# Optimization experiments

Hardware: AMD Instinct MI355X
Metric: run time of the kernel (lower is better)

Reference implementation:

```python
import jax, jax.numpy as jnp
import numpy as np

H, D = 8, 128           # num_heads, head_dim
HID = 1024              # hidden_size
K = 4                   # short conv kernel
EPS_QK = 1e-6
EPS_NORM = 1e-5


def short_conv(x, w):
    # x: (B, T, C), w: (C, 1, K) depthwise causal conv (zero initial state) + SiLU
    k = w.shape[-1]
    xp = jnp.pad(x, ((0, 0), (k - 1, 0), (0, 0)))
    xc = jnp.transpose(xp, (0, 2, 1))  # (B, C, T+K-1)
    y = jax.lax.conv_general_dilated(xc, w, window_strides=(1,), padding='VALID',
                                     feature_group_count=w.shape[0])
    return jax.nn.silu(jnp.transpose(y, (0, 2, 1)))


def _rmsn(t, eps):
    return t * jax.lax.rsqrt(jnp.mean(t * t, axis=-1, keepdims=True) + eps)


def setup_inputs() -> dict:
    key = jax.random.key(0)
    ks = jax.random.split(key, 16)
    s = 0.02
    inp = {
        'x': jax.random.normal(ks[0], (2, 1024, HID), dtype=jnp.float32),
        'Wq': jax.random.normal(ks[1], (H * D, HID), dtype=jnp.float32) * s,
        'Wk': jax.random.normal(ks[2], (H * D, HID), dtype=jnp.float32) * s,
        'Wv': jax.random.normal(ks[3], (H * D, HID), dtype=jnp.float32) * s,
        'wq_conv': jax.random.normal(ks[4], (H * D, 1, K), dtype=jnp.float32) * 0.3,
        'wk_conv': jax.random.normal(ks[5], (H * D, 1, K), dtype=jnp.float32) * 0.3,
        'wv_conv': jax.random.normal(ks[6], (H * D, 1, K), dtype=jnp.float32) * 0.3,
        'Wfa': jax.random.normal(ks[7], (D, HID), dtype=jnp.float32) * s,
        'Wfb': jax.random.normal(ks[8], (H * D, D), dtype=jnp.float32) * s,
        'Wb': jax.random.normal(ks[9], (H, HID), dtype=jnp.float32) * s,
        'Wga': jax.random.normal(ks[10], (D, HID), dtype=jnp.float32) * s,
        'Wgb': jax.random.normal(ks[11], (H * D, D), dtype=jnp.float32) * s,
        'A_log': jnp.log(jax.random.uniform(ks[12], (H,), minval=1.0, maxval=16.0, dtype=jnp.float32)),
        'dt_bias': jnp.zeros((H, D), dtype=jnp.float32),
        'o_norm_w': jnp.ones((D,), dtype=jnp.float32),
        'Wo': jax.random.normal(ks[13], (HID, H * D), dtype=jnp.float32) * s,
    }
    return inp


def reference(x, Wq, Wk, Wv, wq_conv, wk_conv, wv_conv, Wfa, Wfb, Wb, Wga, Wgb,
              A_log, dt_bias, o_norm_w, Wo):
    B, T, _ = x.shape
    scale = float(D) ** -0.5

    q = short_conv(x @ Wq.T, wq_conv).reshape(B, T, H, D)
    k = short_conv(x @ Wk.T, wk_conv).reshape(B, T, H, D)
    v = short_conv(x @ Wv.T, wv_conv).reshape(B, T, H, D)

    q = (scale ** 2) * _rmsn(q, EPS_QK)
    k = scale * _rmsn(k, EPS_QK)

    a_logits = ((x @ Wfa.T) @ Wfb.T).reshape(B, T, H, D)
    g = -jnp.exp(A_log)[None, None, :, None] * jax.nn.softplus(a_logits + dt_bias)  # (B,T,H,D)
    beta = jax.nn.sigmoid(x @ Wb.T)  # (B,T,H)

    # gated delta-rule recurrence over time; state S: (B, H, Dk, Dv)
    def step(S, inputs):
        q_t, k_t, v_t, g_t, b_t = inputs
        S = S * jnp.exp(g_t)[..., None]                       # per-channel decay on key dim
        kv = jnp.einsum('bhd,bhdv->bhv', k_t, S)              # read
        delta = b_t[..., None] * (v_t - kv)                   # beta-gated delta
        S = S + k_t[..., None] * delta[:, :, None, :]         # rank-1 write
        o = jnp.einsum('bhd,bhdv->bhv', q_t, S)
        return S, o

    tb = lambda t: jnp.moveaxis(t, 1, 0)  # (B,T,...) -> (T,B,...)
    S0 = jnp.zeros((B, H, D, D), dtype=x.dtype)
    _, o_t = jax.lax.scan(step, S0, (tb(q), tb(k), tb(v), tb(g), tb(beta)))
    out = jnp.moveaxis(o_t, 0, 1)  # (B, T, H, D)

    gate = ((x @ Wga.T) @ Wgb.T).reshape(B, T, H, D)
    out = _rmsn(out, EPS_NORM) * o_norm_w * jax.nn.sigmoid(gate)
    return out.reshape(B, T, H * D) @ Wo.T
```

## Files before the change

### kernel.cpp

```cpp
#include <hip/hip_runtime.h>
#include <hip/hip_bf16.h>
#include <math.h>

#define H 8
#define D 128
#define HID 1024
#define KCONV 4

typedef __bf16 bhalf;
typedef __bf16 bhalf4 __attribute__((ext_vector_type(4)));
typedef __bf16 bhalf8 __attribute__((ext_vector_type(8)));
typedef float f32x4 __attribute__((ext_vector_type(4)));
typedef _Float16 hlf;
typedef _Float16 half8 __attribute__((ext_vector_type(8)));
typedef _Float16 half4v __attribute__((ext_vector_type(4)));

__device__ __forceinline__ void async16(const void* g, void* l) {
    __builtin_amdgcn_global_load_lds(
        (const __attribute__((address_space(1))) void*)g,
        (__attribute__((address_space(3))) void*)l, 16, 0, 0);
}

__global__ __launch_bounds__(256) void gemm_bf16_nt(const bhalf* A, const bhalf* B,
                                                    void* Cv,
                                                    int M, int N, int K,
                                                    int lda, int ldb, int ldc, int epi,
                                                    const float* __restrict__ A_log,
                                                    const float* __restrict__ dt_bias,
                                                    const bhalf* A2, const bhalf* B2,
                                                    void* C2, int epi2,
                                                    bhalf* __restrict__ pXAG,
                                                    float* __restrict__ pBETA)
{
    if (blockIdx.z) { A = A2; B = B2; Cv = C2; epi = epi2; }
    __shared__ __align__(16) bhalf As[128][32];
    __shared__ __align__(16) bhalf Bs[64][32];
    int tid = threadIdx.x;
    int wid = tid >> 6, lane = tid & 63;
    int rowBase = blockIdx.y * 128;
    int colBase = blockIdx.x * 64;
    int wm = wid >> 1, wn = wid & 1;

    f32x4 acc[4][2] = {};

    int r = lane >> 2;
    int cseg = lane & 3;

    for (int k0 = 0; k0 < K; k0 += 32) {
        __syncthreads();
#pragma unroll
        for (int s = 0; s < 3; ++s) {
            int j = wid * 3 + s;
            if (j < 8) {
                const bhalf* ga = A + (size_t)(rowBase + j * 16 + r) * lda + k0 + cseg * 8;
                async16(ga, &As[j * 16][0]);
            } else {
                int jb = j - 8;
                const bhalf* ga = B + (size_t)(colBase + jb * 16 + r) * ldb + k0 + cseg * 8;
                async16(ga, &Bs[jb * 16][0]);
            }
        }
        __syncthreads();
        int mq = lane & 15, kq = (lane >> 4) * 8;
        bhalf8 af[4], bfr[2];
#pragma unroll
        for (int mt = 0; mt < 4; ++mt)
            af[mt] = *(const bhalf8*)&As[wm * 64 + mt * 16 + mq][kq];
#pragma unroll
        for (int nt = 0; nt < 2; ++nt)
            bfr[nt] = *(const bhalf8*)&Bs[wn * 32 + nt * 16 + mq][kq];
#pragma unroll
        for (int mt = 0; mt < 4; ++mt)
#pragma unroll
            for (int nt = 0; nt < 2; ++nt)
                acc[mt][nt] = __builtin_amdgcn_mfma_f32_16x16x32_bf16(
                    af[mt], bfr[nt], acc[mt][nt], 0, 0, 0);
    }
    int rquad = (lane >> 4) * 4;
#pragma unroll
    for (int mt = 0; mt < 4; ++mt) {
        int m0 = rowBase + wm * 64 + mt * 16 + rquad;
#pragma unroll
        for (int nt = 0; nt < 2; ++nt) {
            int c = colBase + wn * 32 + (lane & 15) + nt * 16;
#pragma unroll
            for (int rr = 0; rr < 4; ++rr) {
                float val = acc[mt][nt][rr];
                int m = m0 + rr;
                if (epi == 0) {
                    ((float*)Cv)[(size_t)m * ldc + c] = val;
                } else if (epi == 1) {
                    int h = c >> 7, d = c & 127;
                    float z = val + dt_bias[h * D + d];
                    float sp = (z > 20.f) ? z : log1pf(expf(z));
                    ((float*)Cv)[(size_t)m * ldc + c] = expf(-expf(A_log[h]) * sp);
                } else if (epi == 2) {
                    ((bhalf*)Cv)[(size_t)m * ldc + c] = (bhalf)val;
                } else {
                    if (c < 3072) {
                        ((float*)Cv)[(size_t)m * 3072 + c] = val;
                    } else if (c < 3328) {
                        pXAG[(size_t)m * 256 + (c - 3072)] = (bhalf)val;
                    } else if (c < 3336) {
                        pBETA[(size_t)m * 8 + (c - 3328)] = 1.f / (1.f + expf(-val));
                    }
                }
            }
        }
    }
}

__global__ void cast1(const float* __restrict__ s, bhalf* __restrict__ d, int n4)
{
    int i = blockIdx.x * blockDim.x + threadIdx.x;
    if (i >= n4) return;
    float4 v = ((const float4*)s)[i];
    bhalf4 o = {(bhalf)v.x, (bhalf)v.y, (bhalf)v.z, (bhalf)v.w};
    ((bhalf4*)d)[i] = o;
}
__global__ void cast4(const float* __restrict__ s0, const float* __restrict__ s1,
                      const float* __restrict__ s2, const float* __restrict__ s3,
                      bhalf* __restrict__ d0, bhalf* __restrict__ d1,
                      bhalf* __restrict__ d2, bhalf* __restrict__ d3, int n4)
{
    int i = blockIdx.x * blockDim.x + threadIdx.x;
    if (i >= n4) return;
    int a = blockIdx.y;
    const float* s = (a == 0) ? s0 : (a == 1) ? s1 : (a == 2) ? s2 : s3;
    bhalf* d = (a == 0) ? d0 : (a == 1) ? d1 : (a == 2) ? d2 : d3;
    float4 v = ((const float4*)s)[i];
    bhalf4 o = {(bhalf)v.x, (bhalf)v.y, (bhalf)v.z, (bhalf)v.w};
    ((bhalf4*)d)[i] = o;
}

__global__ __launch_bounds__(128) void conv3_kernel(const float* __restrict__ QKV,
                                                    const float* __restrict__ wq,
                                                    const float* __restrict__ wk,
                                                    const float* __restrict__ wv,
                                                    float* __restrict__ Qc,
                                                    float* __restrict__ Kc,
                                                    float* __restrict__ Vc,
                                                    int T)
{
    int which = blockIdx.y;
    const float* w; float* out; int mode; float scale;
    if (which == 0)      { w = wq; out = Qc; mode = 1; scale = 1.0f / 128.0f; }
    else if (which == 1) { w = wk; out = Kc; mode = 1; scale = 0.08838834764831845f; }
    else                 { w = wv; out = Vc; mode = 0; scale = 1.f; }

    int bid = blockIdx.x;
    int h = bid % H;
    int t = (bid / H) % T;
    int b = bid / (H * T);
    int d = threadIdx.x;
    int c = h * D + d;
    const float* base = QKV + (size_t)b * T * 3072 + which * 1024 + c;
    float acc = 0.f;
#pragma unroll
    for (int j = 0; j < KCONV; ++j) {
        int tt = t - (KCONV - 1) + j;
        float xv = (tt >= 0) ? base[(size_t)tt * 3072] : 0.f;
        acc += xv * w[c * KCONV + j];
    }
    float y = acc / (1.f + expf(-acc));
    if (mode) {
        __shared__ float red[2];
        float ss = y * y;
#pragma unroll
        for (int s = 32; s > 0; s >>= 1) ss += __shfl_xor(ss, s, 64);
        if ((threadIdx.x & 63) == 0) red[threadIdx.x >> 6] = ss;
        __syncthreads();
        float tot = red[0] + red[1];
        float r = rsqrtf(tot * (1.f / D) + 1e-6f);
        y = y * r * scale;
    }
    out[(size_t)bid * D + d] = y;
}

template <int CTRL>
__device__ __forceinline__ float dpp_add(float x) {
    int y = __builtin_amdgcn_update_dpp(0, __builtin_bit_cast(int, x),
                                        CTRL, 0xF, 0xF, false);
    return x + __builtin_bit_cast(float, y);
}
__device__ __forceinline__ float wave_sum63(float x) {
    x = dpp_add<0x111>(x);
    x = dpp_add<0x112>(x);
    x = dpp_add<0x114>(x);
    x = dpp_add<0x118>(x);
    x = dpp_add<0x142>(x);
    x = dpp_add<0x143>(x);
    return x;
}


__global__ __launch_bounds__(256) void chunk_prep_kernel(
    const float* __restrict__ Q, const float* __restrict__ K,
    const float* __restrict__ V, const float* __restrict__ E,
    const float* __restrict__ BETA,
    hlf* __restrict__ Wn, float* __restrict__ Uf, hlf* __restrict__ Qt,
    hlf* __restrict__ AoL, hlf* __restrict__ KbT, float* __restrict__ Aend,
    int T)
{
    __shared__ __align__(16) float e_s[32][128];
    __shared__ __align__(16) float k_s[32][128];
    __shared__ __align__(16) float U_s[32][128];
    __shared__ __align__(16) hlf  A_s[32][128];
    __shared__ __align__(16) hlf  W_s[32][128];
    __shared__ float P_s[32][32];
    __shared__ float Ao_s[32][32];
    __shared__ float beta_s[32];

    int tid = threadIdx.x, wid = tid >> 6, lane = tid & 63;
    int bid = blockIdx.x;
    int bh = bid >> 5, ch = bid & 31;
    int b = bh >> 3, h = bh & 7;
    int t0 = ch * 32;
    size_t rowb = (size_t)(b * T + t0) * 1024 + h * 128;
    size_t co = (size_t)bh * 32 + ch;

    int rs2 = lane >> 5, seg = (lane & 31) * 4;
#pragma unroll
    for (int p = wid * 4; p < wid * 4 + 4; ++p) {
        int row = p * 2 + rs2;
        async16(E + rowb + (size_t)row * 1024 + seg, &e_s[p * 2][0]);
        async16(K + rowb + (size_t)row * 1024 + seg, &k_s[p * 2][0]);
    }
    __syncthreads();

    for (int x = tid; x < 1024; x += 256) Ao_s[x >> 5][x & 31] = 0.f;
    if (wid == 2 && lane < 32)
        beta_s[lane] = BETA[(size_t)(b * T + t0 + lane) * 8 + h];
    int d0 = lane * 2;
    if (wid == 0) {
        float a0 = 1.f, a1 = 1.f;
        for (int t = 0; t < 32; ++t) {
            a0 *= e_s[t][d0]; a1 *= e_s[t][d0 + 1];
            A_s[t][d0] = (hlf)a0; A_s[t][d0 + 1] = (hlf)a1;
        }
        Aend[co * 128 + d0] = a0; Aend[co * 128 + d0 + 1] = a1;
    } else if (wid == 1) {
        float s0 = 1.f, s1 = 1.f;
        for (int t = 31; t >= 0; --t) {
            KbT[co * 4096 + (size_t)d0 * 32 + t]       = (hlf)(k_s[t][d0] * s0);
            KbT[co * 4096 + (size_t)(d0 + 1) * 32 + t] = (hlf)(k_s[t][d0 + 1] * s1);
            s0 *= e_s[t][d0]; s1 *= e_s[t][d0 + 1];
        }
    }
    __syncthreads();

#pragma unroll
    for (int ii = 0; ii < 8; ++ii) {
        int i = wid + ii * 4;
        float ki0 = k_s[i][d0], ki1 = k_s[i][d0 + 1];
        float2 qv = *(const float2*)(Q + rowb + (size_t)i * 1024 + d0);
        float aa = wave_sum63(qv.x * ki0 + qv.y * ki1);
        if (lane == 63) Ao_s[i][i] = aa;
        float R0 = 1.f, R1 = 1.f;
        for (int j = i - 1; j >= 0; --j) {
            R0 *= e_s[j + 1][d0]; R1 *= e_s[j + 1][d0 + 1];
            float u0 = R0 * k_s[j][d0], u1 = R1 * k_s[j][d0 + 1];
            float pp = wave_sum63(ki0 * u0 + ki1 * u1);
            float a2 = wave_sum63(qv.x * u0 + qv.y * u1);
            if (lane == 63) { P_s[i][j] = pp; Ao_s[i][j] = a2; }
        }
    }
    __syncthreads();

    for (int x = tid; x < 1024; x += 256) {
        int i2 = x >> 5, j2 = x & 31;
        P_s[i2][j2] = (j2 < i2) ? P_s[i2][j2] * beta_s[i2] : 0.f;
    }
    __syncthreads();

    if (wid == 0) {
        for (int i = 0; i < 32; ++i) {
            float bb = beta_s[i];
            float a0 = bb * k_s[i][d0] * (float)A_s[i][d0];
            float a1 = bb * k_s[i][d0 + 1] * (float)A_s[i][d0 + 1];
            for (int k2 = 0; k2 < i; ++k2) {
                float L = P_s[i][k2];
                a0 -= L * (float)W_s[k2][d0];
                a1 -= L * (float)W_s[k2][d0 + 1];
            }
            W_s[i][d0] = (hlf)a0; W_s[i][d0 + 1] = (hlf)a1;
        }
    } else if (wid == 1) {
        for (int i = 0; i < 32; ++i) {
            float bb = beta_s[i];
            float2 vv = *(const float2*)(V + rowb + (size_t)i * 1024 + d0);
            float a0 = bb * vv.x, a1 = bb * vv.y;
            for (int k2 = 0; k2 < i; ++k2) {
                float L = P_s[i][k2];
                a0 -= L * U_s[k2][d0];
                a1 -= L * U_s[k2][d0 + 1];
            }
            U_s[i][d0] = a0; U_s[i][d0 + 1] = a1;
        }
    } else {
        for (int r2 = wid - 2; r2 < 32; r2 += 2) {
            float2 qv = *(const float2*)(Q + rowb + (size_t)r2 * 1024 + d0);
            Qt[co * 4096 + (size_t)r2 * 128 + d0]     = (hlf)(qv.x * (float)A_s[r2][d0]);
            Qt[co * 4096 + (size_t)r2 * 128 + d0 + 1] = (hlf)(qv.y * (float)A_s[r2][d0 + 1]);
        }
    }
    __syncthreads();

    for (int x = tid; x < 4096; x += 256) {
        Wn[co * 4096 + x] = (hlf)(-(float)W_s[x >> 7][x & 127]);
        Uf[co * 4096 + x] = U_s[x >> 7][x & 127];
    }
    for (int x = tid; x < 1024; x += 256)
        AoL[co * 1024 + x] = (hlf)Ao_s[x >> 5][x & 31];
}

__global__ __launch_bounds__(256) void chunk_scan_kernel(
    const hlf* __restrict__ Wn, const float* __restrict__ Uf,
    const hlf* __restrict__ Qt, const hlf* __restrict__ Ao,
    const hlf* __restrict__ KbT, const float* __restrict__ Aend,
    float* __restrict__ O, int T)
{
    __shared__ __align__(16) float Sf[32][132];
    __shared__ __align__(16) hlf  Sh[32][136];
    __shared__ __align__(16) hlf  Dt[32][40];
    __shared__ float Ae[128];

    int tid = threadIdx.x, wid = tid >> 6, lane = tid & 63;
    int nbh = gridDim.x >> 2;
    int bh = blockIdx.x % nbh, vs = blockIdx.x / nbh;
    int b = bh >> 3, h = bh & 7;
    int v0 = vs * 32;

    for (int r = wid; r < 32; r += 4) {
        for (int c2 = lane; c2 < 132; c2 += 64) Sf[r][c2] = 0.f;
        for (int c2 = lane; c2 < 136; c2 += 64) Sh[r][c2] = (hlf)0.f;
    }
    __syncthreads();

    int mq = lane & 15, kq = (lane >> 4) * 8, rq = (lane >> 4) * 4;
    int tr = (wid >> 1) * 16, vc = (wid & 1) * 16;
    int vr2 = (wid >> 1) * 16, dh2 = (wid & 1) * 64;

    for (int c = 0; c < 32; ++c) {
        size_t co = (size_t)bh * 32 + c;
        const hlf*   Wc  = Wn  + co * 4096;
        const float* Uc  = Uf  + co * 4096;
        const hlf*   Qc2 = Qt  + co * 4096;
        const hlf*   Aoc = Ao  + co * 1024;
        const hlf*   Kbc = KbT + co * 4096;
        if (tid < 128) Ae[tid] = Aend[co * 128 + tid];

        f32x4 dacc;
#pragma unroll
        for (int rr = 0; rr < 4; ++rr)
            dacc[rr] = Uc[(size_t)(tr + rq + rr) * 128 + v0 + vc + mq];
#pragma unroll
        for (int ks = 0; ks < 4; ++ks) {
            half8 aw = *(const half8*)&Wc[(size_t)(tr + mq) * 128 + ks * 32 + kq];
            half8 bs = *(const half8*)&Sh[vc + mq][ks * 32 + kq];
            dacc = __builtin_amdgcn_mfma_f32_16x16x32_f16(aw, bs, dacc, 0, 0, 0);
        }
        half4v dh4;
#pragma unroll
        for (int rr = 0; rr < 4; ++rr) dh4[rr] = (hlf)dacc[rr];
        *(half4v*)&Dt[vc + mq][tr + rq] = dh4;
        __syncthreads();

        f32x4 oacc = {0.f, 0.f, 0.f, 0.f};
#pragma unroll
        for (int ks = 0; ks < 4; ++ks) {
            half8 aq = *(const half8*)&Qc2[(size_t)(tr + mq) * 128 + ks * 32 + kq];
            half8 bs = *(const half8*)&Sh[vc + mq][ks * 32 + kq];
            oacc = __builtin_amdgcn_mfma_f32_16x16x32_f16(aq, bs, oacc, 0, 0, 0);
        }
        {
            half8 aA = *(const half8*)&Aoc[(tr + mq) * 32 + kq];
            half8 bD = *(const half8*)&Dt[vc + mq][kq];
            oacc = __builtin_amdgcn_mfma_f32_16x16x32_f16(aA, bD, oacc, 0, 0, 0);
        }
#pragma unroll
        for (int rr = 0; rr < 4; ++rr)
            O[((size_t)(b * T + c * 32 + tr + rq + rr) * 8 + h) * 128 + v0 + vc + mq]
                = oacc[rr];

        f32x4 sacc[4];
        half8 aD = *(const half8*)&Dt[vr2 + mq][kq];
#pragma unroll
        for (int nt = 0; nt < 4; ++nt) {
            int dc = dh2 + nt * 16 + mq;
#pragma unroll
            for (int rr = 0; rr < 4; ++rr)
                sacc[nt][rr] = Sf[vr2 + rq + rr][dc] * Ae[dc];
            half8 bK = *(const half8*)&Kbc[(size_t)dc * 32 + kq];
            sacc[nt] = __builtin_amdgcn_mfma_f32_16x16x32_f16(aD, bK, sacc[nt], 0, 0, 0);
        }
        __syncthreads();
#pragma unroll
        for (int nt = 0; nt < 4; ++nt) {
            int dc = dh2 + nt * 16 + mq;
#pragma unroll
            for (int rr = 0; rr < 4; ++rr) {
                Sf[vr2 + rq + rr][dc] = sacc[nt][rr];
                Sh[vr2 + rq + rr][dc] = (hlf)sacc[nt][rr];
            }
        }
        __syncthreads();
    }
}

__global__ __launch_bounds__(128) void outnorm_kernel(const float* __restrict__ O,
                                                      const float* __restrict__ GATE,
                                                      const float* __restrict__ w,
                                                      bhalf* __restrict__ Obf)
{
    int bid = blockIdx.x;
    int d = threadIdx.x;
    size_t base = (size_t)bid * D;
    float y = O[base + d];
    __shared__ float red[2];
    float ss = y * y;
#pragma unroll
    for (int s = 32; s > 0; s >>= 1) ss += __shfl_xor(ss, s, 64);
    if ((threadIdx.x & 63) == 0) red[threadIdx.x >> 6] = ss;
    __syncthreads();
    float tot = red[0] + red[1];
    float r = rsqrtf(tot * (1.f / D) + 1e-5f);
    float gz = GATE[base + d];
    float sg = 1.f / (1.f + expf(-gz));
    Obf[base + d] = (bhalf)(y * r * w[d] * sg);
}

extern "C" void kernel_launch(void* const* d_in, const int* in_sizes, int n_in,
                              void* d_out, int out_size, void* d_ws, size_t ws_size,
                              hipStream_t stream)
{
    const float* x       = (const float*)d_in[0];
    const float* Wq      = (const float*)d_in[1];
    const float* Wk      = (const float*)d_in[2];
    const float* Wv      = (const float*)d_in[3];
    const float* wq_conv = (const float*)d_in[4];
    const float* wk_conv = (const float*)d_in[5];
    const float* wv_conv = (const float*)d_in[6];
    const float* Wfa     = (const float*)d_in[7];
    const float* Wfb     = (const float*)d_in[8];
    const float* Wb      = (const float*)d_in[9];
    const float* Wga     = (const float*)d_in[10];
    const float* Wgb     = (const float*)d_in[11];
    const float* A_log   = (const float*)d_in[12];
    const float* dt_bias = (const float*)d_in[13];
    const float* o_norm_w= (const float*)d_in[14];
    const float* Wo      = (const float*)d_in[15];

    int BT = in_sizes[0] / HID;
    int T = 1024;
    int B_ = BT / T;
    size_t M = (size_t)BT;
    size_t sz_big = M * HID;
    const int nW = HID * HID;
    const int nS = D * HID;
    const int NCAT = 3392;

    float* fp = (float*)d_ws;
    float* QKVp = fp;               fp += 3 * sz_big;
    float* Qc   = fp;               fp += sz_big;
    float* Kc   = fp;               fp += sz_big;
    float* Vc   = fp;               fp += sz_big;
    float* EGb  = fp;               fp += sz_big;
    float* GATE = fp;               fp += sz_big;
    float* Obuf = fp;               fp += sz_big;
    float* BETA = fp;               fp += M * H;
    bhalf* bp = (bhalf*)fp;
    bhalf* xb   = bp;               bp += sz_big;
    bhalf* Wcat = bp;               bp += (size_t)NCAT * HID;
    bhalf* Wob  = bp;               bp += nW;
    bhalf* Wfbb = bp;               bp += nS;
    bhalf* Wgbb = bp;               bp += nS;
    bhalf* XAG  = bp;               bp += M * 256;
    bhalf* Obf  = bp;               bp += sz_big;

    dim3 blk(256);

    cast1<<<(int)((sz_big / 4 + 255) / 256), 256, 0, stream>>>(x, xb, (int)(sz_big / 4));
    cast4<<<dim3((nW / 4 + 255) / 256, 4), 256, 0, stream>>>(Wq, Wk, Wv, Wo,
        Wcat, Wcat + nW, Wcat + 2 * (size_t)nW, Wob, nW / 4);
    cast4<<<dim3((nS / 4 + 255) / 256, 4), 256, 0, stream>>>(Wfa, Wga, Wfb, Wgb,
        Wcat + 3 * (size_t)nW, Wcat + 3 * (size_t)nW + nS, Wfbb, Wgbb, nS / 4);
    cast1<<<(H * HID / 4 + 255) / 256, 256, 0, stream>>>(Wb,
        Wcat + 3 * (size_t)nW + 2 * (size_t)nS, H * HID / 4);

    gemm_bf16_nt<<<dim3(NCAT / 64, BT / 128), blk, 0, stream>>>(
        xb, Wcat, QKVp, BT, NCAT, HID, HID, HID, 3072, 3, nullptr, nullptr,
        nullptr, nullptr, nullptr, 0, XAG, BETA);

    conv3_kernel<<<dim3(BT * H, 3), 128, 0, stream>>>(QKVp,
                                                      wq_conv, wk_conv, wv_conv,
                                                      Qc, Kc, Vc, T);

    gemm_bf16_nt<<<dim3(HID / 64, BT / 128, 2), blk, 0, stream>>>(
        XAG, Wfbb, EGb, BT, HID, D, 256, D, HID, 1, A_log, dt_bias,
        XAG + D, Wgbb, GATE, 0, nullptr, nullptr);

    int nbh = B_ * 8;
    float* Uf   = QKVp;
    float* Aend = Uf + (size_t)nbh * 32 * 4096;
    hlf* Wn  = (hlf*)(Aend + (size_t)nbh * 32 * 128);
    hlf* Qt  = Wn  + (size_t)nbh * 32 * 4096;
    hlf* AoLp= Qt  + (size_t)nbh * 32 * 4096;
    hlf* KbT = AoLp + (size_t)nbh * 32 * 1024;

    chunk_prep_kernel<<<nbh * 32, 256, 0, stream>>>(Qc, Kc, Vc, EGb, BETA,
                                                    Wn, Uf, Qt, AoLp, KbT, Aend, T);
    chunk_scan_kernel<<<nbh * 4, 256, 0, stream>>>(Wn, Uf, Qt, AoLp, KbT, Aend,
                                                   Obuf, T);

    outnorm_kernel<<<BT * H, 128, 0, stream>>>(Obuf, GATE, o_norm_w, Obf);

    gemm_bf16_nt<<<dim3(HID / 64, BT / 128), blk, 0, stream>>>(
        Obf, Wob, (float*)d_out, BT, HID, HID, HID, HID, HID, 0, nullptr, nullptr,
        nullptr, nullptr, nullptr, 0, nullptr, nullptr);
}
```

Baseline: 331.2 us.

## Prefetch next chunk operands into registers and double-buffer scan state

The chunk scan kernel now loads all global operands for the next chunk into registers while the current chunk computes, and ping-pongs the state between two LDS buffers so one barrier per phase is removed. Barriers become raw s_barrier calls with explicit waitcnt and sched_barrier. The prep kernel also stages Q and V in LDS through async loads instead of reading them from global memory repeatedly. This adds register pressure (launch bounds set to one block per CU) and more LDS use.

```diff
diff --git a/kernel.cpp b/kernel.cpp
--- a/kernel.cpp
+++ b/kernel.cpp
@@ -204,6 +204,8 @@
 {
     __shared__ __align__(16) float e_s[32][128];
     __shared__ __align__(16) float k_s[32][128];
+    __shared__ __align__(16) float q_s[32][128];
+    __shared__ __align__(16) float v_s[32][128];
     __shared__ __align__(16) float U_s[32][128];
     __shared__ __align__(16) hlf  A_s[32][128];
     __shared__ __align__(16) hlf  W_s[32][128];
@@ -225,12 +227,14 @@
         int row = p * 2 + rs2;
         async16(E + rowb + (size_t)row * 1024 + seg, &e_s[p * 2][0]);
         async16(K + rowb + (size_t)row * 1024 + seg, &k_s[p * 2][0]);
-    }
-    __syncthreads();
-
-    for (int x = tid; x < 1024; x += 256) Ao_s[x >> 5][x & 31] = 0.f;
+        async16(Q + rowb + (size_t)row * 1024 + seg, &q_s[p * 2][0]);
+        async16(V + rowb + (size_t)row * 1024 + seg, &v_s[p * 2][0]);
+    }
     if (wid == 2 && lane < 32)
         beta_s[lane] = BETA[(size_t)(b * T + t0 + lane) * 8 + h];
+    __syncthreads();
+
+    for (int x = tid; x < 1024; x += 256) Ao_s[x >> 5][x & 31] = 0.f;
     int d0 = lane * 2;
     if (wid == 0) {
         float a0 = 1.f, a1 = 1.f;
@@ -253,7 +257,7 @@
     for (int ii = 0; ii < 8; ++ii) {
         int i = wid + ii * 4;
         float ki0 = k_s[i][d0], ki1 = k_s[i][d0 + 1];
-        float2 qv = *(const float2*)(Q + rowb + (size_t)i * 1024 + d0);
+        float2 qv = *(const float2*)&q_s[i][d0];
         float aa = wave_sum63(qv.x * ki0 + qv.y * ki1);
         if (lane == 63) Ao_s[i][i] = aa;
         float R0 = 1.f, R1 = 1.f;
@@ -288,7 +292,7 @@
     } else if (wid == 1) {
         for (int i = 0; i < 32; ++i) {
             float bb = beta_s[i];
-            float2 vv = *(const float2*)(V + rowb + (size_t)i * 1024 + d0);
+            float2 vv = *(const float2*)&v_s[i][d0];
             float a0 = bb * vv.x, a1 = bb * vv.y;
             for (int k2 = 0; k2 < i; ++k2) {
                 float L = P_s[i][k2];
@@ -299,7 +303,7 @@
         }
     } else {
         for (int r2 = wid - 2; r2 < 32; r2 += 2) {
-            float2 qv = *(const float2*)(Q + rowb + (size_t)r2 * 1024 + d0);
+            float2 qv = *(const float2*)&q_s[r2][d0];
             Qt[co * 4096 + (size_t)r2 * 128 + d0]     = (hlf)(qv.x * (float)A_s[r2][d0]);
             Qt[co * 4096 + (size_t)r2 * 128 + d0 + 1] = (hlf)(qv.y * (float)A_s[r2][d0 + 1]);
         }
@@ -314,16 +318,123 @@
         AoL[co * 1024 + x] = (hlf)Ao_s[x >> 5][x & 31];
 }
 
-__global__ __launch_bounds__(256) void chunk_scan_kernel(
+struct ScanOps {
+    half8 aw0, aw1, aw2, aw3;
+    half8 aq0, aq1, aq2, aq3;
+    half8 bK0, bK1, bK2, bK3;
+    half8 aA;
+    float u0, u1, u2, u3;
+    float ae0, ae1, ae2, ae3;
+};
+
+__device__ __forceinline__ void scan_load(ScanOps& o, size_t co,
+    const hlf* __restrict__ Wn, const float* __restrict__ Uf,
+    const hlf* __restrict__ Qt, const hlf* __restrict__ Ao,
+    const hlf* __restrict__ KbT, const float* __restrict__ Aend,
+    int tr, int vc, int dh2, int mq, int kq, int rq, int v0)
+{
+    const hlf*   Wc  = Wn  + co * 4096;
+    const hlf*   Qc  = Qt  + co * 4096;
+    const hlf*   Aoc = Ao  + co * 1024;
+    const hlf*   Kbc = KbT + co * 4096;
+    const float* Uc  = Uf  + co * 4096;
+    const float* Aec = Aend + co * 128;
+    size_t rw = (size_t)(tr + mq) * 128 + kq;
+    o.aw0 = *(const half8*)&Wc[rw];
+    o.aw1 = *(const half8*)&Wc[rw + 32];
+    o.aw2 = *(const half8*)&Wc[rw + 64];
+    o.aw3 = *(const half8*)&Wc[rw + 96];
+    o.aq0 = *(const half8*)&Qc[rw];
+    o.aq1 = *(const half8*)&Qc[rw + 32];
+    o.aq2 = *(const half8*)&Qc[rw + 64];
+    o.aq3 = *(const half8*)&Qc[rw + 96];
+    o.aA  = *(const half8*)&Aoc[(tr + mq) * 32 + kq];
+    o.bK0 = *(const half8*)&Kbc[(size_t)(dh2 + mq) * 32 + kq];
+    o.bK1 = *(const half8*)&Kbc[(size_t)(dh2 + 16 + mq) * 32 + kq];
+    o.bK2 = *(const half8*)&Kbc[(size_t)(dh2 + 32 + mq) * 32 + kq];
+    o.bK3 = *(const half8*)&Kbc[(size_t)(dh2 + 48 + mq) * 32 + kq];
+    size_t ru = (size_t)(tr + rq) * 128 + v0 + vc + mq;
+    o.u0 = Uc[ru];
+    o.u1 = Uc[ru + 128];
+    o.u2 = Uc[ru + 256];
+    o.u3 = Uc[ru + 384];
+    o.ae0 = Aec[dh2 + mq];
+    o.ae1 = Aec[dh2 + 16 + mq];
+    o.ae2 = Aec[dh2 + 32 + mq];
+    o.ae3 = Aec[dh2 + 48 + mq];
+}
+
+__device__ __forceinline__ void scan_body(const ScanOps& o, int c,
+    float (*SfR)[132], hlf (*ShR)[136], float (*SfW)[132], hlf (*ShW)[136],
+    hlf (*Dt)[40], float* __restrict__ O,
+    int b, int h, int v0, int T,
+    int tr, int vc, int vr2, int dh2, int mq, int kq, int rq)
+{
+    half8 bs0 = *(const half8*)&ShR[vc + mq][kq];
+    half8 bs1 = *(const half8*)&ShR[vc + mq][32 + kq];
+    half8 bs2 = *(const half8*)&ShR[vc + mq][64 + kq];
+    half8 bs3 = *(const half8*)&ShR[vc + mq][96 + kq];
+
+    f32x4 dacc = {o.u0, o.u1, o.u2, o.u3};
+    dacc = __builtin_amdgcn_mfma_f32_16x16x32_f16(o.aw0, bs0, dacc, 0, 0, 0);
+    dacc = __builtin_amdgcn_mfma_f32_16x16x32_f16(o.aw1, bs1, dacc, 0, 0, 0);
+    dacc = __builtin_amdgcn_mfma_f32_16x16x32_f16(o.aw2, bs2, dacc, 0, 0, 0);
+    dacc = __builtin_amdgcn_mfma_f32_16x16x32_f16(o.aw3, bs3, dacc, 0, 0, 0);
+    half4v dh4 = {(hlf)dacc[0], (hlf)dacc[1], (hlf)dacc[2], (hlf)dacc[3]};
+    *(half4v*)&Dt[vc + mq][tr + rq] = dh4;
+
+    asm volatile("s_waitcnt lgkmcnt(0)" ::: "memory");
+    __builtin_amdgcn_s_barrier();
+    __builtin_amdgcn_sched_barrier(0);
+
+    f32x4 oacc = {0.f, 0.f, 0.f, 0.f};
+    oacc = __builtin_amdgcn_mfma_f32_16x16x32_f16(o.aq0, bs0, oacc, 0, 0, 0);
+    oacc = __builtin_amdgcn_mfma_f32_16x16x32_f16(o.aq1, bs1, oacc, 0, 0, 0);
+    oacc = __builtin_amdgcn_mfma_f32_16x16x32_f16(o.aq2, bs2, oacc, 0, 0, 0);
+    oacc = __builtin_amdgcn_mfma_f32_16x16x32_f16(o.aq3, bs3, oacc, 0, 0, 0);
+    half8 bD = *(const half8*)&Dt[vc + mq][kq];
+    oacc = __builtin_amdgcn_mfma_f32_16x16x32_f16(o.aA, bD, oacc, 0, 0, 0);
+    size_t ob = ((size_t)(b * T + c * 32 + tr + rq) * 8 + h) * 128 + v0 + vc + mq;
+    O[ob]        = oacc[0];
+    O[ob + 1024] = oacc[1];
+    O[ob + 2048] = oacc[2];
+    O[ob + 3072] = oacc[3];
+
+    half8 aD = *(const half8*)&Dt[vr2 + mq][kq];
+    int dc0 = dh2 + mq, dc1 = dh2 + 16 + mq, dc2 = dh2 + 32 + mq, dc3 = dh2 + 48 + mq;
+    f32x4 s0, s1, s2, s3;
+#pragma unroll
+    for (int rr = 0; rr < 4; ++rr) {
+        s0[rr] = SfR[vr2 + rq + rr][dc0] * o.ae0;
+        s1[rr] = SfR[vr2 + rq + rr][dc1] * o.ae1;
+        s2[rr] = SfR[vr2 + rq + rr][dc2] * o.ae2;
+        s3[rr] = SfR[vr2 + rq + rr][dc3] * o.ae3;
+    }
+    s0 = __builtin_amdgcn_mfma_f32_16x16x32_f16(aD, o.bK0, s0, 0, 0, 0);
+    s1 = __builtin_amdgcn_mfma_f32_16x16x32_f16(aD, o.bK1, s1, 0, 0, 0);
+    s2 = __builtin_amdgcn_mfma_f32_16x16x32_f16(aD, o.bK2, s2, 0, 0, 0);
+    s3 = __builtin_amdgcn_mfma_f32_16x16x32_f16(aD, o.bK3, s3, 0, 0, 0);
+#pragma unroll
+    for (int rr = 0; rr < 4; ++rr) {
+        SfW[vr2 + rq + rr][dc0] = s0[rr];  ShW[vr2 + rq + rr][dc0] = (hlf)s0[rr];
+        SfW[vr2 + rq + rr][dc1] = s1[rr];  ShW[vr2 + rq + rr][dc1] = (hlf)s1[rr];
+        SfW[vr2 + rq + rr][dc2] = s2[rr];  ShW[vr2 + rq + rr][dc2] = (hlf)s2[rr];
+        SfW[vr2 + rq + rr][dc3] = s3[rr];  ShW[vr2 + rq + rr][dc3] = (hlf)s3[rr];
+    }
+    asm volatile("s_waitcnt lgkmcnt(0)" ::: "memory");
+    __builtin_amdgcn_s_barrier();
+    __builtin_amdgcn_sched_barrier(0);
+}
+
+__global__ __launch_bounds__(256, 1) void chunk_scan_kernel(
     const hlf* __restrict__ Wn, const float* __restrict__ Uf,
     const hlf* __restrict__ Qt, const hlf* __restrict__ Ao,
     const hlf* __restrict__ KbT, const float* __restrict__ Aend,
     float* __restrict__ O, int T)
 {
-    __shared__ __align__(16) float Sf[32][132];
-    __shared__ __align__(16) hlf  Sh[32][136];
+    __shared__ __align__(16) float Sf0[32][132], Sf1[32][132];
+    __shared__ __align__(16) hlf  Sh0[32][136], Sh1[32][136];
     __shared__ __align__(16) hlf  Dt[32][40];
-    __shared__ float Ae[128];
 
     int tid = threadIdx.x, wid = tid >> 6, lane = tid & 63;
     int nbh = gridDim.x >> 2;
@@ -332,79 +443,30 @@
     int v0 = vs * 32;
 
     for (int r = wid; r < 32; r += 4) {
-        for (int c2 = lane; c2 < 132; c2 += 64) Sf[r][c2] = 0.f;
-        for (int c2 = lane; c2 < 136; c2 += 64) Sh[r][c2] = (hlf)0.f;
-    }
-    __syncthreads();
+        for (int c2 = lane; c2 < 132; c2 += 64) Sf0[r][c2] = 0.f;
+        for (int c2 = lane; c2 < 136; c2 += 64) Sh0[r][c2] = (hlf)0.f;
+    }
 
     int mq = lane & 15, kq = (lane >> 4) * 8, rq = (lane >> 4) * 4;
     int tr = (wid >> 1) * 16, vc = (wid & 1) * 16;
     int vr2 = (wid >> 1) * 16, dh2 = (wid & 1) * 64;
 
-    for (int c = 0; c < 32; ++c) {
-        size_t co = (size_t)bh * 32 + c;
-        const hlf*   Wc  = Wn  + co * 4096;
-        const float* Uc  = Uf  + co * 4096;
-        const hlf*   Qc2 = Qt  + co * 4096;
-        const hlf*   Aoc = Ao  + co * 1024;
-        const hlf*   Kbc = KbT + co * 4096;
-        if (tid < 128) Ae[tid] = Aend[co * 128 + tid];
-
-        f32x4 dacc;
-#pragma unroll
-        for (int rr = 0; rr < 4; ++rr)
-            dacc[rr] = Uc[(size_t)(tr + rq + rr) * 128 + v0 + vc + mq];
-#pragma unroll
-        for (int ks = 0; ks < 4; ++ks) {
-            half8 aw = *(const half8*)&Wc[(size_t)(tr + mq) * 128 + ks * 32 + kq];
-            half8 bs = *(const half8*)&Sh[vc + mq][ks * 32 + kq];
-            dacc = __builtin_amdgcn_mfma_f32_16x16x32_f16(aw, bs, dacc, 0, 0, 0);
-        }
-        half4v dh4;
-#pragma unroll
-        for (int rr = 0; rr < 4; ++rr) dh4[rr] = (hlf)dacc[rr];
-        *(half4v*)&Dt[vc + mq][tr + rq] = dh4;
-        __syncthreads();
-
-        f32x4 oacc = {0.f, 0.f, 0.f, 0.f};
-#pragma unroll
-        for (int ks = 0; ks < 4; ++ks) {
-            half8 aq = *(const half8*)&Qc2[(size_t)(tr + mq) * 128 + ks * 32 + kq];
-            half8 bs = *(const half8*)&Sh[vc + mq][ks * 32 + kq];
-            oacc = __builtin_amdgcn_mfma_f32_16x16x32_f16(aq, bs, oacc, 0, 0, 0);
-        }
-        {
-            half8 aA = *(const half8*)&Aoc[(tr + mq) * 32 + kq];
-            half8 bD = *(const half8*)&Dt[vc + mq][kq];
-            oacc = __builtin_amdgcn_mfma_f32_16x16x32_f16(aA, bD, oacc, 0, 0, 0);
-        }
-#pragma unroll
-        for (int rr = 0; rr < 4; ++rr)
-            O[((size_t)(b * T + c * 32 + tr + rq + rr) * 8 + h) * 128 + v0 + vc + mq]
-                = oacc[rr];
-
-        f32x4 sacc[4];
-        half8 aD = *(const half8*)&Dt[vr2 + mq][kq];
-#pragma unroll
-        for (int nt = 0; nt < 4; ++nt) {
-            int dc = dh2 + nt * 16 + mq;
-#pragma unroll
-            for (int rr = 0; rr < 4; ++rr)
-                sacc[nt][rr] = Sf[vr2 + rq + rr][dc] * Ae[dc];
-            half8 bK = *(const half8*)&Kbc[(size_t)dc * 32 + kq];
-            sacc[nt] = __builtin_amdgcn_mfma_f32_16x16x32_f16(aD, bK, sacc[nt], 0, 0, 0);
-        }
-        __syncthreads();
-#pragma unroll
-        for (int nt = 0; nt < 4; ++nt) {
-            int dc = dh2 + nt * 16 + mq;
-#pragma unroll
-            for (int rr = 0; rr < 4; ++rr) {
-                Sf[vr2 + rq + rr][dc] = sacc[nt][rr];
-                Sh[vr2 + rq + rr][dc] = (hlf)sacc[nt][rr];
-            }
-        }
-        __syncthreads();
+    int NC = T / 32;
+    size_t cb = (size_t)bh * 32;
+    ScanOps opA, opB;
+    scan_load(opA, cb, Wn, Uf, Qt, Ao, KbT, Aend, tr, vc, dh2, mq, kq, rq, v0);
+    __syncthreads();
+
+    for (int cc = 0; cc < NC; cc += 2) {
+        scan_load(opB, cb + cc + 1, Wn, Uf, Qt, Ao, KbT, Aend,
+                  tr, vc, dh2, mq, kq, rq, v0);
+        scan_body(opA, cc, Sf0, Sh0, Sf1, Sh1, Dt, O, b, h, v0, T,
+                  tr, vc, vr2, dh2, mq, kq, rq);
+        if (cc + 2 < NC)
+            scan_load(opA, cb + cc + 2, Wn, Uf, Qt, Ao, KbT, Aend,
+                      tr, vc, dh2, mq, kq, rq, v0);
+        scan_body(opB, cc + 1, Sf1, Sh1, Sf0, Sh0, Dt, O, b, h, v0, T,
+                  tr, vc, vr2, dh2, mq, kq, rq);
     }
 }
 
```

Result: slower. 352.3 us (+6.4%).

## Rewrite chunk scan as single-wave blocks with register state and double-buffered prefetch

Applied to the files above, without the earlier changes.

Rewrites the chunk scan kernel so each block is one wavefront that owns a 16-column slice of the value dimension, raising the grid from 4 to 8 blocks per (batch, head). The fp32 state now lives in registers instead of LDS. Operands for the next two chunks are prefetched with inline-asm global loads and async LDS copies, with manual waitcnt control, removing block-wide barriers from the sequential chunk loop. The output buffer moves to a slice-major layout that outnorm now indexes, and the prep kernel stages V through LDS asynchronously. The cost is heavy register pressure, fragile hand-tuned wait counts, and one wave per block.

```diff
diff --git a/kernel.cpp b/kernel.cpp
--- a/kernel.cpp
+++ b/kernel.cpp
@@ -225,6 +225,7 @@
         int row = p * 2 + rs2;
         async16(E + rowb + (size_t)row * 1024 + seg, &e_s[p * 2][0]);
         async16(K + rowb + (size_t)row * 1024 + seg, &k_s[p * 2][0]);
+        async16(V + rowb + (size_t)row * 1024 + seg, &U_s[p * 2][0]);
     }
     __syncthreads();
 
@@ -288,7 +289,7 @@
     } else if (wid == 1) {
         for (int i = 0; i < 32; ++i) {
             float bb = beta_s[i];
-            float2 vv = *(const float2*)(V + rowb + (size_t)i * 1024 + d0);
+            float2 vv = *(const float2*)&U_s[i][d0];
             float a0 = bb * vv.x, a1 = bb * vv.y;
             for (int k2 = 0; k2 < i; ++k2) {
                 float L = P_s[i][k2];
@@ -314,109 +315,262 @@
         AoL[co * 1024 + x] = (hlf)Ao_s[x >> 5][x & 31];
 }
 
-__global__ __launch_bounds__(256) void chunk_scan_kernel(
+struct ScanOpsA {
+    half8 aw0, aw1, aw2, aw3, aw4, aw5, aw6, aw7;
+    half8 aq0, aq1, aq2, aq3, aq4, aq5, aq6, aq7;
+    half8 aA0, aA1;
+    float u0, u1, u2, u3, u4, u5, u6, u7;
+};
+
+#define GLOAD16(dst, ptr) \
+    asm volatile("global_load_dwordx4 %0, %1, off" : "=v"(dst) : "v"(ptr))
+#define GLOAD4(dst, ptr) \
+    asm volatile("global_load_dword %0, %1, off" : "=v"(dst) : "v"(ptr))
+
+#define SCAN_WAIT35(o) \
+    do { \
+    asm volatile("s_waitcnt vmcnt(35)" \
+        : "+v"(o.aw0), "+v"(o.aw1), "+v"(o.aw2), "+v"(o.aw3), \
+          "+v"(o.aw4), "+v"(o.aw5), "+v"(o.aw6), "+v"(o.aw7), \
+          "+v"(o.aq0), "+v"(o.aq1), "+v"(o.aq2), "+v"(o.aq3), \
+          "+v"(o.aq4), "+v"(o.aq5), "+v"(o.aq6), "+v"(o.aq7) \
+        :: "memory"); \
+    asm volatile("" \
+        : "+v"(o.aA0), "+v"(o.aA1), \
+          "+v"(o.u0), "+v"(o.u1), "+v"(o.u2), "+v"(o.u3), \
+          "+v"(o.u4), "+v"(o.u5), "+v"(o.u6), "+v"(o.u7)); \
+    __builtin_amdgcn_sched_barrier(0); \
+    } while (0)
+
+__device__ __forceinline__ void scan_loadA(ScanOpsA& o, size_t co,
+    const hlf* __restrict__ Wn, const float* __restrict__ Uf,
+    const hlf* __restrict__ Qt, const hlf* __restrict__ Ao,
+    int mq, int kq, int rq, int v0)
+{
+    const hlf*   Wc  = Wn + co * 4096;
+    const hlf*   Qc  = Qt + co * 4096;
+    const hlf*   Aoc = Ao + co * 1024;
+    const float* Uc  = Uf + co * 4096;
+    size_t rw0 = (size_t)mq * 128 + kq;
+    size_t rw1 = (size_t)(16 + mq) * 128 + kq;
+    GLOAD16(o.aw0, &Wc[rw0]);
+    GLOAD16(o.aw1, &Wc[rw0 + 32]);
+    GLOAD16(o.aw2, &Wc[rw0 + 64]);
+    GLOAD16(o.aw3, &Wc[rw0 + 96]);
+    GLOAD16(o.aw4, &Wc[rw1]);
+    GLOAD16(o.aw5, &Wc[rw1 + 32]);
+    GLOAD16(o.aw6, &Wc[rw1 + 64]);
+    GLOAD16(o.aw7, &Wc[rw1 + 96]);
+    GLOAD16(o.aq0, &Qc[rw0]);
+    GLOAD16(o.aq1, &Qc[rw0 + 32]);
+    GLOAD16(o.aq2, &Qc[rw0 + 64]);
+    GLOAD16(o.aq3, &Qc[rw0 + 96]);
+    GLOAD16(o.aq4, &Qc[rw1]);
+    GLOAD16(o.aq5, &Qc[rw1 + 32]);
+    GLOAD16(o.aq6, &Qc[rw1 + 64]);
+    GLOAD16(o.aq7, &Qc[rw1 + 96]);
+    GLOAD16(o.aA0, &Aoc[mq * 32 + kq]);
+    GLOAD16(o.aA1, &Aoc[(16 + mq) * 32 + kq]);
+    size_t ru0 = (size_t)rq * 128 + v0 + mq;
+    size_t ru1 = (size_t)(16 + rq) * 128 + v0 + mq;
+    GLOAD4(o.u0, &Uc[ru0]);
+    GLOAD4(o.u1, &Uc[ru0 + 128]);
+    GLOAD4(o.u2, &Uc[ru0 + 256]);
+    GLOAD4(o.u3, &Uc[ru0 + 384]);
+    GLOAD4(o.u4, &Uc[ru1]);
+    GLOAD4(o.u5, &Uc[ru1 + 128]);
+    GLOAD4(o.u6, &Uc[ru1 + 256]);
+    GLOAD4(o.u7, &Uc[ru1 + 384]);
+}
+
+__device__ __forceinline__ void scan_stage(size_t co,
+    const hlf* __restrict__ KbT, const float* __restrict__ Aend,
+    hlf* kbt_l, float* ae_l, int lane)
+{
+    const hlf* Kbc = KbT + co * 4096;
+#pragma unroll
+    for (int p = 0; p < 8; ++p)
+        async16(Kbc + p * 512 + lane * 8, kbt_l + p * 512);
+    async16(Aend + co * 128 + lane * 4, ae_l);
+}
+
+__device__ __forceinline__ void scan_body(const ScanOpsA& o,
+    const hlf* kbt_l, const float* ae_l, int c,
+    f32x4* sreg, half8* Sb, hlf (*Sh)[136], hlf (*Dt)[40],
+    float* __restrict__ O, int b, int h, int vs, int T, int Mrows,
+    int mq, int kq, int rq)
+{
+    f32x4 d0 = {0.f, 0.f, 0.f, 0.f}, d1 = {0.f, 0.f, 0.f, 0.f};
+    d0 = __builtin_amdgcn_mfma_f32_16x16x32_f16(o.aw0, Sb[0], d0, 0, 0, 0);
+    d0 = __builtin_amdgcn_mfma_f32_16x16x32_f16(o.aw1, Sb[1], d0, 0, 0, 0);
+    d0 = __builtin_amdgcn_mfma_f32_16x16x32_f16(o.aw2, Sb[2], d0, 0, 0, 0);
+    d0 = __builtin_amdgcn_mfma_f32_16x16x32_f16(o.aw3, Sb[3], d0, 0, 0, 0);
+    d1 = __builtin_amdgcn_mfma_f32_16x16x32_f16(o.aw4, Sb[0], d1, 0, 0, 0);
+    d1 = __builtin_amdgcn_mfma_f32_16x16x32_f16(o.aw5, Sb[1], d1, 0, 0, 0);
+    d1 = __builtin_amdgcn_mfma_f32_16x16x32_f16(o.aw6, Sb[2], d1, 0, 0, 0);
+    d1 = __builtin_amdgcn_mfma_f32_16x16x32_f16(o.aw7, Sb[3], d1, 0, 0, 0);
+    d0[0] += o.u0; d0[1] += o.u1; d0[2] += o.u2; d0[3] += o.u3;
+    d1[0] += o.u4; d1[1] += o.u5; d1[2] += o.u6; d1[3] += o.u7;
+    half4v dh0 = {(hlf)d0[0], (hlf)d0[1], (hlf)d0[2], (hlf)d0[3]};
+    half4v dh1 = {(hlf)d1[0], (hlf)d1[1], (hlf)d1[2], (hlf)d1[3]};
+    *(half4v*)&Dt[mq][rq]      = dh0;
+    *(half4v*)&Dt[mq][16 + rq] = dh1;
+
+    f32x4 o0 = {0.f, 0.f, 0.f, 0.f}, o1 = {0.f, 0.f, 0.f, 0.f};
+    o0 = __builtin_amdgcn_mfma_f32_16x16x32_f16(o.aq0, Sb[0], o0, 0, 0, 0);
+    o0 = __builtin_amdgcn_mfma_f32_16x16x32_f16(o.aq1, Sb[1], o0, 0, 0, 0);
+    o0 = __builtin_amdgcn_mfma_f32_16x16x32_f16(o.aq2, Sb[2], o0, 0, 0, 0);
+    o0 = __builtin_amdgcn_mfma_f32_16x16x32_f16(o.aq3, Sb[3], o0, 0, 0, 0);
+    o1 = __builtin_amdgcn_mfma_f32_16x16x32_f16(o.aq4, Sb[0], o1, 0, 0, 0);
+    o1 = __builtin_amdgcn_mfma_f32_16x16x32_f16(o.aq5, Sb[1], o1, 0, 0, 0);
+    o1 = __builtin_amdgcn_mfma_f32_16x16x32_f16(o.aq6, Sb[2], o1, 0, 0, 0);
+    o1 = __builtin_amdgcn_mfma_f32_16x16x32_f16(o.aq7, Sb[3], o1, 0, 0, 0);
+
+    asm volatile("s_waitcnt lgkmcnt(0)" ::: "memory");
+    __builtin_amdgcn_sched_barrier(0);
+
+    half8 Dtb = *(const half8*)&Dt[mq][kq];
+    o0 = __builtin_amdgcn_mfma_f32_16x16x32_f16(o.aA0, Dtb, o0, 0, 0, 0);
+    o1 = __builtin_amdgcn_mfma_f32_16x16x32_f16(o.aA1, Dtb, o1, 0, 0, 0);
+    size_t ob = (size_t)vs * Mrows * 128 +
+                ((size_t)(b * T + c * 32 + rq) * 8 + h) * 16 + mq;
+    O[ob]       = o0[0];
+    O[ob + 128] = o0[1];
+    O[ob + 256] = o0[2];
+    O[ob + 384] = o0[3];
+    size_t ob1 = ob + 2048;
+    O[ob1]       = o1[0];
+    O[ob1 + 128] = o1[1];
+    O[ob1 + 256] = o1[2];
+    O[ob1 + 384] = o1[3];
+
+    half8 bk0 = *(const half8*)&kbt_l[(size_t)(mq) * 32 + kq];
+    half8 bk1 = *(const half8*)&kbt_l[(size_t)(16 + mq) * 32 + kq];
+    half8 bk2 = *(const half8*)&kbt_l[(size_t)(32 + mq) * 32 + kq];
+    half8 bk3 = *(const half8*)&kbt_l[(size_t)(48 + mq) * 32 + kq];
+    half8 bk4 = *(const half8*)&kbt_l[(size_t)(64 + mq) * 32 + kq];
+    half8 bk5 = *(const half8*)&kbt_l[(size_t)(80 + mq) * 32 + kq];
+    half8 bk6 = *(const half8*)&kbt_l[(size_t)(96 + mq) * 32 + kq];
+    half8 bk7 = *(const half8*)&kbt_l[(size_t)(112 + mq) * 32 + kq];
+    f32x4 ae0 = *(const f32x4*)&ae_l[rq];
+    f32x4 ae1 = *(const f32x4*)&ae_l[16 + rq];
+    f32x4 ae2 = *(const f32x4*)&ae_l[32 + rq];
+    f32x4 ae3 = *(const f32x4*)&ae_l[48 + rq];
+    f32x4 ae4 = *(const f32x4*)&ae_l[64 + rq];
+    f32x4 ae5 = *(const f32x4*)&ae_l[80 + rq];
+    f32x4 ae6 = *(const f32x4*)&ae_l[96 + rq];
+    f32x4 ae7 = *(const f32x4*)&ae_l[112 + rq];
+    f32x4 s0 = sreg[0] * ae0;
+    f32x4 s1 = sreg[1] * ae1;
+    f32x4 s2 = sreg[2] * ae2;
+    f32x4 s3 = sreg[3] * ae3;
+    f32x4 s4 = sreg[4] * ae4;
+    f32x4 s5 = sreg[5] * ae5;
+    f32x4 s6 = sreg[6] * ae6;
+    f32x4 s7 = sreg[7] * ae7;
+    s0 = __builtin_amdgcn_mfma_f32_16x16x32_f16(bk0, Dtb, s0, 0, 0, 0);
+    s1 = __builtin_amdgcn_mfma_f32_16x16x32_f16(bk1, Dtb, s1, 0, 0, 0);
+    s2 = __builtin_amdgcn_mfma_f32_16x16x32_f16(bk2, Dtb, s2, 0, 0, 0);
+    s3 = __builtin_amdgcn_mfma_f32_16x16x32_f16(bk3, Dtb, s3, 0, 0, 0);
+    s4 = __builtin_amdgcn_mfma_f32_16x16x32_f16(bk4, Dtb, s4, 0, 0, 0);
+    s5 = __builtin_amdgcn_mfma_f32_16x16x32_f16(bk5, Dtb, s5, 0, 0, 0);
+    s6 = __builtin_amdgcn_mfma_f32_16x16x32_f16(bk6, Dtb, s6, 0, 0, 0);
+    s7 = __builtin_amdgcn_mfma_f32_16x16x32_f16(bk7, Dtb, s7, 0, 0, 0);
+    sreg[0] = s0; sreg[1] = s1; sreg[2] = s2; sreg[3] = s3;
+    sreg[4] = s4; sreg[5] = s5; sreg[6] = s6; sreg[7] = s7;
+    {
+        half4v h0 = {(hlf)s0[0], (hlf)s0[1], (hlf)s0[2], (hlf)s0[3]};
+        half4v h1 = {(hlf)s1[0], (hlf)s1[1], (hlf)s1[2], (hlf)s1[3]};
+        half4v h2 = {(hlf)s2[0], (hlf)s2[1], (hlf)s2[2], (hlf)s2[3]};
+        half4v h3 = {(hlf)s3[0], (hlf)s3[1], (hlf)s3[2], (hlf)s3[3]};
+        half4v h4 = {(hlf)s4[0], (hlf)s4[1], (hlf)s4[2], (hlf)s4[3]};
+        half4v h5 = {(hlf)s5[0], (hlf)s5[1], (hlf)s5[2], (hlf)s5[3]};
+        half4v h6 = {(hlf)s6[0], (hlf)s6[1], (hlf)s6[2], (hlf)s6[3]};
+        half4v h7 = {(hlf)s7[0], (hlf)s7[1], (hlf)s7[2], (hlf)s7[3]};
+        *(half4v*)&Sh[mq][rq]        = h0;
+        *(half4v*)&Sh[mq][16 + rq]   = h1;
+        *(half4v*)&Sh[mq][32 + rq]   = h2;
+        *(half4v*)&Sh[mq][48 + rq]   = h3;
+        *(half4v*)&Sh[mq][64 + rq]   = h4;
+        *(half4v*)&Sh[mq][80 + rq]   = h5;
+        *(half4v*)&Sh[mq][96 + rq]   = h6;
+        *(half4v*)&Sh[mq][112 + rq]  = h7;
+    }
+    asm volatile("s_waitcnt lgkmcnt(0)" ::: "memory");
+    __builtin_amdgcn_sched_barrier(0);
+    Sb[0] = *(const half8*)&Sh[mq][kq];
+    Sb[1] = *(const half8*)&Sh[mq][32 + kq];
+    Sb[2] = *(const half8*)&Sh[mq][64 + kq];
+    Sb[3] = *(const half8*)&Sh[mq][96 + kq];
+    asm volatile("s_waitcnt lgkmcnt(0)" ::: "memory");
+    __builtin_amdgcn_sched_barrier(0);
+}
+
+__global__ __launch_bounds__(64, 1) void chunk_scan_kernel(
     const hlf* __restrict__ Wn, const float* __restrict__ Uf,
     const hlf* __restrict__ Qt, const hlf* __restrict__ Ao,
     const hlf* __restrict__ KbT, const float* __restrict__ Aend,
     float* __restrict__ O, int T)
 {
-    __shared__ __align__(16) float Sf[32][132];
-    __shared__ __align__(16) hlf  Sh[32][136];
-    __shared__ __align__(16) hlf  Dt[32][40];
-    __shared__ float Ae[128];
-
-    int tid = threadIdx.x, wid = tid >> 6, lane = tid & 63;
-    int nbh = gridDim.x >> 2;
+    __shared__ __align__(16) hlf  kbt_l[2][4096];
+    __shared__ __align__(16) float ae_l[2][256];
+    __shared__ __align__(16) hlf  Sh[16][136];
+    __shared__ __align__(16) hlf  Dt[16][40];
+
+    int lane = threadIdx.x & 63;
+    int nbh = gridDim.x >> 3;
     int bh = blockIdx.x % nbh, vs = blockIdx.x / nbh;
     int b = bh >> 3, h = bh & 7;
-    int v0 = vs * 32;
-
-    for (int r = wid; r < 32; r += 4) {
-        for (int c2 = lane; c2 < 132; c2 += 64) Sf[r][c2] = 0.f;
-        for (int c2 = lane; c2 < 136; c2 += 64) Sh[r][c2] = (hlf)0.f;
-    }
-    __syncthreads();
+    int v0 = vs * 16;
+    int Mrows = (nbh >> 3) * T;
 
     int mq = lane & 15, kq = (lane >> 4) * 8, rq = (lane >> 4) * 4;
-    int tr = (wid >> 1) * 16, vc = (wid & 1) * 16;
-    int vr2 = (wid >> 1) * 16, dh2 = (wid & 1) * 64;
-
-    for (int c = 0; c < 32; ++c) {
-        size_t co = (size_t)bh * 32 + c;
-        const hlf*   Wc  = Wn  + co * 4096;
-        const float* Uc  = Uf  + co * 4096;
-        const hlf*   Qc2 = Qt  + co * 4096;
-        const hlf*   Aoc = Ao  + co * 1024;
-        const hlf*   Kbc = KbT + co * 4096;
-        if (tid < 128) Ae[tid] = Aend[co * 128 + tid];
-
-        f32x4 dacc;
-#pragma unroll
-        for (int rr = 0; rr < 4; ++rr)
-            dacc[rr] = Uc[(size_t)(tr + rq + rr) * 128 + v0 + vc + mq];
-#pragma unroll
-        for (int ks = 0; ks < 4; ++ks) {
-            half8 aw = *(const half8*)&Wc[(size_t)(tr + mq) * 128 + ks * 32 + kq];
-            half8 bs = *(const half8*)&Sh[vc + mq][ks * 32 + kq];
-            dacc = __builtin_amdgcn_mfma_f32_16x16x32_f16(aw, bs, dacc, 0, 0, 0);
-        }
-        half4v dh4;
-#pragma unroll
-        for (int rr = 0; rr < 4; ++rr) dh4[rr] = (hlf)dacc[rr];
-        *(half4v*)&Dt[vc + mq][tr + rq] = dh4;
-        __syncthreads();
-
-        f32x4 oacc = {0.f, 0.f, 0.f, 0.f};
-#pragma unroll
-        for (int ks = 0; ks < 4; ++ks) {
-            half8 aq = *(const half8*)&Qc2[(size_t)(tr + mq) * 128 + ks * 32 + kq];
-            half8 bs = *(const half8*)&Sh[vc + mq][ks * 32 + kq];
-            oacc = __builtin_amdgcn_mfma_f32_16x16x32_f16(aq, bs, oacc, 0, 0, 0);
-        }
-        {
-            half8 aA = *(const half8*)&Aoc[(tr + mq) * 32 + kq];
-            half8 bD = *(const half8*)&Dt[vc + mq][kq];
-            oacc = __builtin_amdgcn_mfma_f32_16x16x32_f16(aA, bD, oacc, 0, 0, 0);
-        }
-#pragma unroll
-        for (int rr = 0; rr < 4; ++rr)
-            O[((size_t)(b * T + c * 32 + tr + rq + rr) * 8 + h) * 128 + v0 + vc + mq]
-                = oacc[rr];
-
-        f32x4 sacc[4];
-        half8 aD = *(const half8*)&Dt[vr2 + mq][kq];
-#pragma unroll
-        for (int nt = 0; nt < 4; ++nt) {
-            int dc = dh2 + nt * 16 + mq;
-#pragma unroll
-            for (int rr = 0; rr < 4; ++rr)
-                sacc[nt][rr] = Sf[vr2 + rq + rr][dc] * Ae[dc];
-            half8 bK = *(const half8*)&Kbc[(size_t)dc * 32 + kq];
-            sacc[nt] = __builtin_amdgcn_mfma_f32_16x16x32_f16(aD, bK, sacc[nt], 0, 0, 0);
-        }
-        __syncthreads();
-#pragma unroll
-        for (int nt = 0; nt < 4; ++nt) {
-            int dc = dh2 + nt * 16 + mq;
-#pragma unroll
-            for (int rr = 0; rr < 4; ++rr) {
-                Sf[vr2 + rq + rr][dc] = sacc[nt][rr];
-                Sh[vr2 + rq + rr][dc] = (hlf)sacc[nt][rr];
-            }
-        }
-        __syncthreads();
-    }
+
+    f32x4 sreg[8] = {};
+    half8 Sb[4];
+    half8 hz = {(hlf)0.f, (hlf)0.f, (hlf)0.f, (hlf)0.f,
+                (hlf)0.f, (hlf)0.f, (hlf)0.f, (hlf)0.f};
+    Sb[0] = hz; Sb[1] = hz; Sb[2] = hz; Sb[3] = hz;
+
+    int NC = T / 32;
+    size_t cb = (size_t)bh * 32;
+    size_t comax = (size_t)nbh * 32 - 1;
+
+    ScanOpsA op0, op1;
+    scan_loadA(op0, cb, Wn, Uf, Qt, Ao, mq, kq, rq, v0);
+    scan_stage(cb, KbT, Aend, &kbt_l[0][0], &ae_l[0][0], lane);
+    scan_loadA(op1, cb + 1, Wn, Uf, Qt, Ao, mq, kq, rq, v0);
+    scan_stage(cb + 1, KbT, Aend, &kbt_l[1][0], &ae_l[1][0], lane);
+
+#define CCLAMP(x) ((x) > comax ? comax : (x))
+    for (int cc = 0; cc < NC; cc += 2) {
+        SCAN_WAIT35(op0);
+        scan_body(op0, &kbt_l[0][0], &ae_l[0][0], cc, sreg, Sb, Sh, Dt, O,
+                  b, h, vs, T, Mrows, mq, kq, rq);
+        scan_loadA(op0, CCLAMP(cb + cc + 2), Wn, Uf, Qt, Ao, mq, kq, rq, v0);
+        scan_stage(CCLAMP(cb + cc + 2), KbT, Aend,
+                   &kbt_l[0][0], &ae_l[0][0], lane);
+
+        SCAN_WAIT35(op1);
+        scan_body(op1, &kbt_l[1][0], &ae_l[1][0], cc + 1, sreg, Sb, Sh, Dt, O,
+                  b, h, vs, T, Mrows, mq, kq, rq);
+        scan_loadA(op1, CCLAMP(cb + cc + 3), Wn, Uf, Qt, Ao, mq, kq, rq, v0);
+        scan_stage(CCLAMP(cb + cc + 3), KbT, Aend,
+                   &kbt_l[1][0], &ae_l[1][0], lane);
+    }
+#undef CCLAMP
 }
 
 __global__ __launch_bounds__(128) void outnorm_kernel(const float* __restrict__ O,
                                                       const float* __restrict__ GATE,
                                                       const float* __restrict__ w,
-                                                      bhalf* __restrict__ Obf)
+                                                      bhalf* __restrict__ Obf,
+                                                      int Mrows)
 {
     int bid = blockIdx.x;
     int d = threadIdx.x;
     size_t base = (size_t)bid * D;
-    float y = O[base + d];
+    float y = O[(size_t)(d >> 4) * Mrows * 128 + (size_t)bid * 16 + (d & 15)];
     __shared__ float red[2];
     float ss = y * y;
 #pragma unroll
@@ -510,10 +664,10 @@
 
     chunk_prep_kernel<<<nbh * 32, 256, 0, stream>>>(Qc, Kc, Vc, EGb, BETA,
                                                     Wn, Uf, Qt, AoLp, KbT, Aend, T);
-    chunk_scan_kernel<<<nbh * 4, 256, 0, stream>>>(Wn, Uf, Qt, AoLp, KbT, Aend,
-                                                   Obuf, T);
-
-    outnorm_kernel<<<BT * H, 128, 0, stream>>>(Obuf, GATE, o_norm_w, Obf);
+    chunk_scan_kernel<<<nbh * 8, 64, 0, stream>>>(Wn, Uf, Qt, AoLp, KbT, Aend,
+                                                  Obuf, T);
+
+    outnorm_kernel<<<BT * H, 128, 0, stream>>>(Obuf, GATE, o_norm_w, Obf, BT);
 
     gemm_bf16_nt<<<dim3(HID / 64, BT / 128), blk, 0, stream>>>(
         Obf, Wob, (float*)d_out, BT, HID, HID, HID, HID, HID, 0, nullptr, nullptr,
```

Result: faster. 305.5 us (-7.8%).
